# Performance work log

Measured on AMD Instinct MI355X. Metric: run time of the kernel, lower is better.

The kernel has to match this reference:

```python
import jax, jax.numpy as jnp
import numpy as np

N, E, V, H, HEADS, L, B = 20000, 320000, 100, 128, 3, 2, 200
NEG = 0.2   # leaky_relu negative_slope
EPS = 1e-5  # LayerNorm eps


def _mean_nodes(x, gid):
    # dgl.mean_nodes: per-graph mean of node features
    s = jax.ops.segment_sum(x, gid, num_segments=B)
    c = jax.ops.segment_sum(jnp.ones((x.shape[0], 1), x.dtype), gid, num_segments=B)
    return s / jnp.maximum(c, 1.0)


def _gat_layer(h, src, dst, Wn, bn, att, Ws, b, gamma, beta):
    # weight_node: Linear(H, H*HEADS)
    wv = (h @ Wn + bn).reshape(-1, HEADS, H)
    u = wv[src]  # [E, heads, H] gathered src features
    # attn = leaky_relu(sum(cat(u, v) * w_att)) split into u/v halves (no concat materialized)
    attn = (jnp.einsum('ehd,hd->eh', u, att[:, :H])
            + jnp.einsum('ehd,hd->eh', wv[dst], att[:, H:]))
    attn = jax.nn.leaky_relu(attn, NEG)  # [E, heads]
    # segment softmax over incoming edges of each dst node (mailbox softmax)
    m = jax.ops.segment_max(attn, dst, num_segments=N)
    m = jnp.where(jnp.isfinite(m), m, 0.0)
    e = jnp.exp(attn - m[dst])
    s = jax.ops.segment_sum(e, dst, num_segments=N)
    score = e / s[dst]
    agg = jax.ops.segment_sum(score[:, :, None] * u, dst, num_segments=N)  # [N, heads, H]
    res = agg.reshape(-1, HEADS * H) @ Ws + b
    # DGL leaves zero-in-degree nodes with zero reduced features (reduce_func never runs)
    has_in = jax.ops.segment_sum(jnp.ones((E,), h.dtype), dst, num_segments=N) > 0
    res = jnp.where(has_in[:, None], res, 0.0)
    x = res + h  # residual, then LayerNorm, relu (dropout is eval-mode identity)
    mu = jnp.mean(x, -1, keepdims=True)
    var = jnp.var(x, -1, keepdims=True)
    x = (x - mu) * jax.lax.rsqrt(var + EPS) * gamma + beta
    return jax.nn.relu(x)


def _gru_dir(x, Wih, Whh, bih, bhh, reverse):
    # torch nn.GRU single direction; x: [B, T, in]
    def step(hprev, xt):
        gi = xt @ Wih.T + bih
        gh = hprev @ Whh.T + bhh
        ir, iz, inn = jnp.split(gi, 3, -1)
        hr, hz, hn = jnp.split(gh, 3, -1)
        r = jax.nn.sigmoid(ir + hr)
        z = jax.nn.sigmoid(iz + hz)
        n = jnp.tanh(inn + r * hn)
        hnew = (1.0 - z) * n + z * hprev
        return hnew, hnew
    h0 = jnp.zeros((x.shape[0], Whh.shape[1]), x.dtype)
    hT, ys = jax.lax.scan(step, h0, jnp.swapaxes(x, 0, 1), reverse=reverse)
    return jnp.swapaxes(ys, 0, 1), hT


def setup_inputs() -> dict:
    key = jax.random.key(0)
    k = jax.random.split(key, 16)
    sc = 0.05
    return {
        'h': jax.random.normal(k[0], (N, H), jnp.float32),
        'wid': jax.random.randint(k[1], (N,), 0, V),
        'src': jax.random.randint(k[2], (E,), 0, N),
        'dst': jax.random.randint(k[3], (E,), 0, N),
        'graph_ids': jnp.sort(jax.random.randint(k[4], (N,), 0, B)),
        'proj_W': jax.random.normal(k[5], (V + H, H), jnp.float32) * sc,
        'proj_b': jnp.zeros((H,), jnp.float32),
        'conv_Wn': jax.random.normal(k[6], (L, H, HEADS * H), jnp.float32) * sc,
        'conv_bn': jnp.zeros((L, HEADS * H), jnp.float32),
        'conv_att': jax.random.normal(k[7], (L, HEADS, 2 * H), jnp.float32) * sc,
        'conv_Ws': jax.random.normal(k[8], (L, HEADS * H, H), jnp.float32) * sc,
        'conv_b': jnp.zeros((L, H), jnp.float32),
        'conv_gamma': jnp.ones((L, H), jnp.float32),
        'conv_beta': jnp.zeros((L, H), jnp.float32),
        'gru_Wih0': jax.random.normal(k[9], (2, 3 * H, H), jnp.float32) * sc,
        'gru_Whh0': jax.random.normal(k[10], (2, 3 * H, H), jnp.float32) * sc,
        'gru_bih0': jnp.zeros((2, 3 * H), jnp.float32),
        'gru_bhh0': jnp.zeros((2, 3 * H), jnp.float32),
        'gru_Wih1': jax.random.normal(k[11], (2, 3 * H, 2 * H), jnp.float32) * sc,
        'gru_Whh1': jax.random.normal(k[12], (2, 3 * H, H), jnp.float32) * sc,
        'gru_bih1': jnp.zeros((2, 3 * H), jnp.float32),
        'gru_bhh1': jnp.zeros((2, 3 * H), jnp.float32),
    }


def reference(h, wid, src, dst, graph_ids, proj_W, proj_b, conv_Wn, conv_bn, conv_att, conv_Ws, conv_b, conv_gamma, conv_beta, gru_Wih0, gru_Whh0, gru_bih0, gru_bhh0, gru_Wih1, gru_Whh1, gru_bih1, gru_bhh1):
    one_hot = jax.nn.one_hot(wid, V, dtype=h.dtype)
    hcur = jnp.concatenate([one_hot, h], -1) @ proj_W + proj_b  # project
    readouts = [_mean_nodes(hcur, graph_ids)]
    for l in range(L):
        hcur = _gat_layer(hcur, src, dst, conv_Wn[l], conv_bn[l], conv_att[l],
                          conv_Ws[l], conv_b[l], conv_gamma[l], conv_beta[l])
        readouts.append(_mean_nodes(hcur, graph_ids))
    x = jnp.stack(readouts, 1)  # [B, L+1, H] GRU readout sequence
    finals = []
    for (Wih, Whh, bih, bhh) in ((gru_Wih0, gru_Whh0, gru_bih0, gru_bhh0),
                                 (gru_Wih1, gru_Whh1, gru_bih1, gru_bhh1)):
        yf, hf = _gru_dir(x, Wih[0], Whh[0], bih[0], bhh[0], False)
        yb, hb = _gru_dir(x, Wih[1], Whh[1], bih[1], bhh[1], True)
        x = jnp.concatenate([yf, yb], -1)
        finals += [hf, hb]
    # torch returns h_n [num_layers*2, B, H]; module takes mean over dim 0
    return jnp.mean(jnp.stack(finals, 0), 0)  # [B, H]
```

## Files before the change

kernel.cpp:

```cpp
#include <hip/hip_runtime.h>
#include <cstddef>

static constexpr int Nn    = 20000;
static constexpr int Ee    = 320000;
static constexpr int Vv    = 100;
static constexpr int Hh    = 128;
static constexpr int HEADS = 3;
static constexpr int Bb    = 200;
static constexpr float NEG = 0.2f;
static constexpr float EPS = 1e-5f;

typedef short bf16x8 __attribute__((ext_vector_type(8)));
typedef float f32x4  __attribute__((ext_vector_type(4)));

__device__ inline unsigned short bf16_rne(float x) {
    unsigned u = __builtin_bit_cast(unsigned, x);
    u += 0x7FFFu + ((u >> 16) & 1u);
    return (unsigned short)(u >> 16);
}
__device__ inline float bf16_f(unsigned short h) {
    unsigned u = ((unsigned)h) << 16;
    return __builtin_bit_cast(float, u);
}
__device__ inline float bf_lo(unsigned u) { return __builtin_bit_cast(float, u << 16); }
__device__ inline float bf_hi(unsigned u) { return __builtin_bit_cast(float, u & 0xFFFF0000u); }
__device__ inline float lrelu(float a) { return a >= 0.f ? a : NEG * a; }
__device__ inline float sigmoidf(float x) { return 1.f / (1.f + __expf(-x)); }

__global__ void hist_dst(const int* __restrict__ dst, int* __restrict__ deg) {
    for (int i = blockIdx.x * blockDim.x + threadIdx.x; i < Ee; i += gridDim.x * blockDim.x)
        atomicAdd(&deg[dst[i]], 1);
}

__global__ __launch_bounds__(1024) void scan_offsets(const int* __restrict__ deg,
                                                     int* __restrict__ offs,
                                                     int* __restrict__ cur) {
    __shared__ int sums[1024];
    const int tid = threadIdx.x;
    const int per = (Nn + 1023) >> 10;
    int begin = tid * per;
    int end = begin + per; if (end > Nn) end = Nn;
    if (begin > Nn) begin = Nn;
    int s = 0;
    for (int i = begin; i < end; i++) s += deg[i];
    sums[tid] = s;
    __syncthreads();
    for (int off = 1; off < 1024; off <<= 1) {
// ... 7 lines not shown
        offs[i] = run; cur[i] = run;
        run += deg[i];
    }
    if (end == Nn) offs[Nn] = run;
}

__global__ void fill_csr(const int* __restrict__ dst, const int* __restrict__ src,
                         int* __restrict__ cur, int* __restrict__ csrc) {
    for (int i = blockIdx.x * blockDim.x + threadIdx.x; i < Ee; i += gridDim.x * blockDim.x) {
        int p = atomicAdd(&cur[dst[i]], 1);
        csrc[p] = src[i];
    }
}

struct PrepArgs {
    const float *projW, *convWn, *convWs, *Wih0, *Whh0, *Wih1, *Whh1;
    const int* gid;
    unsigned short *pBth, *pBtl;
    unsigned short *WnTh0, *WnTl0, *WnTh1, *WnTl1;
    unsigned short *WsTh0, *WsTl0, *WsTh1, *WsTl1;
    float *WihT0, *WhhT0, *WihT1, *WhhT1;
    int* goffs;
};

__device__ inline void wsplit(const float* B, int K, int N, int idx,
                              unsigned short* Bth, unsigned short* Btl) {
    int k = idx / N, n = idx - k * N;
    float v = B[idx];
    unsigned short h = bf16_rne(v);
    unsigned short l = bf16_rne(v - bf16_f(h));
    Bth[(size_t)n * K + k] = h;
    Btl[(size_t)n * K + k] = l;
}
__device__ inline void gruT(const float* W, int K, int idx, float* WT) {
    int d = idx / (384 * K);
    int r = idx - d * 384 * K;
    int j = r / K, k = r - j * K;
    WT[(size_t)d * K * 384 + (size_t)k * 384 + j] = W[idx];
}

__global__ void prep_all(PrepArgs a) {
    int i = blockIdx.x * blockDim.x + threadIdx.x;
    if (i < 16384)  { wsplit(a.projW, 128, 128, i, a.pBth, a.pBtl); return; }   i -= 16384;
    if (i < 49152)  { wsplit(a.convWn, 128, 384, i, a.WnTh0, a.WnTl0); return; } i -= 49152;
    if (i < 49152)  { wsplit(a.convWn + 49152, 128, 384, i, a.WnTh1, a.WnTl1); return; } i -= 49152;
    if (i < 49152)  { wsplit(a.convWs, 384, 128, i, a.WsTh0, a.WsTl0); return; } i -= 49152;
    if (i < 49152)  { wsplit(a.convWs + 49152, 384, 128, i, a.WsTh1, a.WsTl1); return; } i -= 49152;
    if (i < 98304)  { gruT(a.Wih0, 128, i, a.WihT0); return; }  i -= 98304;
    if (i < 98304)  { gruT(a.Whh0, 128, i, a.WhhT0); return; }  i -= 98304;
    if (i < 196608) { gruT(a.Wih1, 256, i, a.WihT1); return; }  i -= 196608;
    if (i < 98304)  { gruT(a.Whh1, 128, i, a.WhhT1); return; }  i -= 98304;
    if (i < Nn) {
        int g = a.gid[i];
        if (i == 0) { for (int b = 0; b <= g; b++) a.goffs[b] = 0; }
        else { int pg = a.gid[i - 1]; for (int b = pg + 1; b <= g; b++) a.goffs[b] = i; }
        if (i == Nn - 1) { for (int b = g + 1; b <= Bb; b++) a.goffs[b] = Nn; }
    }
}

struct GArgs {
    const float* A; const unsigned short* Bth; const unsigned short* Btl;
    const float* bias; int M, N, K;
    const int* wid; const float* projW;
    unsigned short* Cb; float* adf; float* addf; const float* att;
    const int* deg; const float* gamma; const float* beta;
    float* hcur;
    const int* gid; float* reado;
};

template <int MODE>
__global__ __launch_bounds__(256) void gemm_fused(GArgs a) {
    constexpr int WM = (MODE == 1) ? 2 : 1;
    constexpr int WN = 4 / WM;
    constexpr int MI = 2;
    constexpr int NI = (MODE == 1) ? 4 : 2;
    constexpr int BM = WM * MI * 16;
    __shared__ unsigned short As_hi[BM][40];
    __shared__ unsigned short As_lo[BM][40];
    __shared__ unsigned short Bs_hi[128][40];
    __shared__ unsigned short Bs_lo[128][40];
    const int tid  = threadIdx.x;
    const int row0 = blockIdx.y * BM;
    const int col0 = blockIdx.x * 128;
    const int w    = tid >> 6;
    const int wm   = w / WN;
    const int wn   = w % WN;
    const int L    = tid & 63;
    const int lrow = L & 15;
    const int lq   = L >> 4;
    const int M = a.M, N = a.N, K = a.K;

    f32x4 acc[MI][NI];
#pragma unroll
    for (int i = 0; i < MI; i++)
#pragma unroll
        for (int j = 0; j < NI; j++) acc[i][j] = (f32x4){0.f, 0.f, 0.f, 0.f};

    for (int kb = 0; kb < K; kb += 32) {
#pragma unroll
        for (int it = 0; it < BM / 32; it++) {
            int idx = tid + it * 256;
            int m  = idx >> 3;
            int kq = (idx & 7) * 4;
            int gr = row0 + m;
            float4 v = make_float4(0.f, 0.f, 0.f, 0.f);
            if (gr < M) v = *(const float4*)(a.A + (size_t)gr * K + kb + kq);
            unsigned short h0 = bf16_rne(v.x), h1 = bf16_rne(v.y),
                           h2 = bf16_rne(v.z), h3 = bf16_rne(v.w);
            short4 hi4 = make_short4((short)h0, (short)h1, (short)h2, (short)h3);
            short4 lo4 = make_short4((short)bf16_rne(v.x - bf16_f(h0)),
                                     (short)bf16_rne(v.y - bf16_f(h1)),
                                     (short)bf16_rne(v.z - bf16_f(h2)),
                                     (short)bf16_rne(v.w - bf16_f(h3)));
            *(short4*)&As_hi[m][kq] = hi4;
            *(short4*)&As_lo[m][kq] = lo4;
        }
        {
            int n  = tid >> 1;
            int kh = (tid & 1) * 16;
            const unsigned short* sh = a.Bth + (size_t)(col0 + n) * K + kb + kh;
            const unsigned short* sl = a.Btl + (size_t)(col0 + n) * K + kb + kh;
            *(float4*)&Bs_hi[n][kh]     = *(const float4*)sh;
            *(float4*)&Bs_hi[n][kh + 8] = *(const float4*)(sh + 8);
            *(float4*)&Bs_lo[n][kh]     = *(const float4*)sl;
            *(float4*)&Bs_lo[n][kh + 8] = *(const float4*)(sl + 8);
        }
        __syncthreads();
        bf16x8 ah[MI], al[MI], bh[NI], bl[NI];
#pragma unroll
        for (int mi = 0; mi < MI; mi++) {
            int r = wm * 32 + mi * 16 + lrow;
            ah[mi] = *(const bf16x8*)&As_hi[r][lq * 8];
            al[mi] = *(const bf16x8*)&As_lo[r][lq * 8];
        }
#pragma unroll
        for (int ni = 0; ni < NI; ni++) {
            int r = wn * NI * 16 + ni * 16 + lrow;
            bh[ni] = *(const bf16x8*)&Bs_hi[r][lq * 8];
            bl[ni] = *(const bf16x8*)&Bs_lo[r][lq * 8];
        }
#pragma unroll
        for (int mi = 0; mi < MI; mi++)
#pragma unroll
            for (int ni = 0; ni < NI; ni++) {
                acc[mi][ni] = __builtin_amdgcn_mfma_f32_16x16x32_bf16(ah[mi], bh[ni], acc[mi][ni], 0, 0, 0);
                acc[mi][ni] = __builtin_amdgcn_mfma_f32_16x16x32_bf16(ah[mi], bl[ni], acc[mi][ni], 0, 0, 0);
                acc[mi][ni] = __builtin_amdgcn_mfma_f32_16x16x32_bf16(al[mi], bh[ni], acc[mi][ni], 0, 0, 0);
            }
        __syncthreads();
    }

    float b4[NI];
#pragma unroll
    for (int ni = 0; ni < NI; ni++)
        b4[ni] = a.bias ? a.bias[col0 + wn * NI * 16 + ni * 16 + lrow] : 0.f;
#pragma unroll
    for (int mi = 0; mi < MI; mi++)
#pragma unroll
        for (int ni = 0; ni < NI; ni++)
#pragma unroll
            for (int r = 0; r < 4; r++) acc[mi][ni][r] += b4[ni];

    if constexpr (MODE == 0) {
        __shared__ float ytile[32][132];
        __shared__ int sgid[32];
#pragma unroll
        for (int mi = 0; mi < MI; mi++)
#pragma unroll
            for (int r = 0; r < 4; r++) {
                int lr = mi * 16 + lq * 4 + r;
                int row = row0 + lr;
                int wi = a.wid[row];
#pragma unroll
                for (int ni = 0; ni < NI; ni++) {
                    int c = wn * 32 + ni * 16 + lrow;
                    float y = acc[mi][ni][r] + a.projW[(size_t)wi * 128 + c];
                    a.hcur[(size_t)row * 128 + c] = y;
                    ytile[lr][c] = y;
                }
            }
        if (tid < 32) sgid[tid] = a.gid[row0 + tid];
        __syncthreads();
        int j = tid & 127, hh = tid >> 7;
        float sum = 0.f; int curg = -1;
        for (int r = hh * 16; r < hh * 16 + 16; r++) {
            int g = sgid[r];
            if (g != curg) {
                if (curg >= 0) atomicAdd(&a.reado[(size_t)curg * 128 + j], sum);
                sum = 0.f; curg = g;
            }
            sum += ytile[r][j];
        }
        if (curg >= 0) atomicAdd(&a.reado[(size_t)curg * 128 + j], sum);
    }

    if constexpr (MODE == 1) {
#pragma unroll
        for (int mi = 0; mi < MI; mi++)
#pragma unroll
            for (int ni = 0; ni < NI; ni++) {
                int col = col0 + wn * 64 + ni * 16 + lrow;
#pragma unroll
                for (int r = 0; r < 4; r++) {
                    int row = row0 + wm * 32 + mi * 16 + lq * 4 + r;
                    if (row < M) a.Cb[(size_t)row * N + col] = bf16_rne(acc[mi][ni][r]);
                }
            }
        const int h = blockIdx.x;
        const float* attS = a.att + h * 256;
        const float* attD = attS + 128;
        __shared__ float sred[64][2], dred[64][2];
        float as4[NI], ad4[NI];
#pragma unroll
        for (int ni = 0; ni < NI; ni++) {
            int cl = wn * 64 + ni * 16 + lrow;
            as4[ni] = attS[cl]; ad4[ni] = attD[cl];
        }
#pragma unroll
        for (int mi = 0; mi < MI; mi++)
#pragma unroll
            for (int r = 0; r < 4; r++) {
                float ps = 0.f, pd = 0.f;
#pragma unroll
                for (int ni = 0; ni < NI; ni++) {
                    ps += acc[mi][ni][r] * as4[ni];
                    pd += acc[mi][ni][r] * ad4[ni];
                }
#pragma unroll
                for (int o = 1; o < 16; o <<= 1) {
                    ps += __shfl_xor(ps, o, 64);
                    pd += __shfl_xor(pd, o, 64);
                }
                if (lrow == 0) {
                    int lr = wm * 32 + mi * 16 + lq * 4 + r;
                    sred[lr][wn] = ps; dred[lr][wn] = pd;
                }
            }
        __syncthreads();
        if (tid < 64) {
            int row = row0 + tid;
            if (row < M) {
                a.adf[(size_t)row * 4 + h]  = sred[tid][0] + sred[tid][1];
                a.addf[(size_t)row * 4 + h] = dred[tid][0] + dred[tid][1];
            }
        }
    }

    if constexpr (MODE == 2) {
        __shared__ float red1[32][4], red2[32][4];
        __shared__ float ytile[32][132];
        __shared__ int sgid[32];
        float g4[NI], be4[NI];
#pragma unroll
        for (int ni = 0; ni < NI; ni++) {
            int c = wn * 32 + ni * 16 + lrow;
            g4[ni] = a.gamma[c]; be4[ni] = a.beta[c];
        }
#pragma unroll
        for (int mi = 0; mi < MI; mi++)
#pragma unroll
            for (int r = 0; r < 4; r++) {
                int lr = mi * 16 + lq * 4 + r;
                int row = row0 + lr;
                int dg = a.deg[row];
#pragma unroll
                for (int ni = 0; ni < NI; ni++) {
                    int c = wn * 32 + ni * 16 + lrow;
                    float hold = a.hcur[(size_t)row * 128 + c];
                    acc[mi][ni][r] = hold + (dg > 0 ? acc[mi][ni][r] : 0.f);
                }
            }
#pragma unroll
        for (int mi = 0; mi < MI; mi++)
#pragma unroll
            for (int r = 0; r < 4; r++) {
                float ps = acc[mi][0][r] + acc[mi][1][r];
#pragma unroll
                for (int o = 1; o < 16; o <<= 1) ps += __shfl_xor(ps, o, 64);
                if (lrow == 0) red1[mi * 16 + lq * 4 + r][wn] = ps;
            }
        __syncthreads();
#pragma unroll
        for (int mi = 0; mi < MI; mi++)
#pragma unroll
            for (int r = 0; r < 4; r++) {
                int lr = mi * 16 + lq * 4 + r;
                float mu = (red1[lr][0] + red1[lr][1] + red1[lr][2] + red1[lr][3]) * (1.f / 128.f);
                float qs = 0.f;
#pragma unroll
                for (int ni = 0; ni < NI; ni++) {
                    float dx = acc[mi][ni][r] - mu;
                    qs += dx * dx;
                }
#pragma unroll
                for (int o = 1; o < 16; o <<= 1) qs += __shfl_xor(qs, o, 64);
                if (lrow == 0) red2[lr][wn] = qs;
            }
        __syncthreads();
#pragma unroll
        for (int mi = 0; mi < MI; mi++)
#pragma unroll
            for (int r = 0; r < 4; r++) {
                int lr = mi * 16 + lq * 4 + r;
                int row = row0 + lr;
                float mu = (red1[lr][0] + red1[lr][1] + red1[lr][2] + red1[lr][3]) * (1.f / 128.f);
                float var = (red2[lr][0] + red2[lr][1] + red2[lr][2] + red2[lr][3]) * (1.f / 128.f);
                float rs = rsqrtf(var + EPS);
#pragma unroll
                for (int ni = 0; ni < NI; ni++) {
                    int c = wn * 32 + ni * 16 + lrow;
                    float y = fmaxf((acc[mi][ni][r] - mu) * rs * g4[ni] + be4[ni], 0.f);
                    a.hcur[(size_t)row * 128 + c] = y;
                    ytile[lr][c] = y;
                }
            }
        if (tid < 32) sgid[tid] = a.gid[row0 + tid];
        __syncthreads();
        int j = tid & 127, hh = tid >> 7;
        float sum = 0.f; int curg = -1;
        for (int r = hh * 16; r < hh * 16 + 16; r++) {
            int g = sgid[r];
            if (g != curg) {
                if (curg >= 0) atomicAdd(&a.reado[(size_t)curg * 128 + j], sum);
                sum = 0.f; curg = g;
            }
            sum += ytile[r][j];
        }
        if (curg >= 0) atomicAdd(&a.reado[(size_t)curg * 128 + j], sum);
    }
}

__global__ __launch_bounds__(256) void gat_aggregate(const unsigned short* __restrict__ wv,
                                                     const float4* __restrict__ ad,
                                                     const float4* __restrict__ add,
                                                     const int* __restrict__ offs,
                                                     const int* __restrict__ csrc,
                                                     float* __restrict__ agg) {
    const int n = (blockIdx.x * 256 + threadIdx.x) >> 6;
    const int L = threadIdx.x & 63;
    if (n >= Nn) return;
    const int start = offs[n];
    const int deg = offs[n + 1] - start;
    float2* o2 = (float2*)(agg + (size_t)n * 384);
    if (deg == 0) {
        float2 z = make_float2(0.f, 0.f);
        o2[L] = z; o2[64 + L] = z; o2[128 + L] = z;
        return;
    }
    const float4 adn = add[n];
    float m0 = -1e30f, m1 = -1e30f, m2 = -1e30f;
    float s0 = 0.f, s1 = 0.f, s2 = 0.f;
    for (int i = L; i < deg; i += 64) {
        int sn = csrc[start + i];
        float4 a4 = ad[sn];
        float a0 = lrelu(a4.x + adn.x);
        float a1 = lrelu(a4.y + adn.y);
        float a2 = lrelu(a4.z + adn.z);
        float nm;
        nm = fmaxf(m0, a0); s0 = s0 * __expf(m0 - nm) + __expf(a0 - nm); m0 = nm;
        nm = fmaxf(m1, a1); s1 = s1 * __expf(m1 - nm) + __expf(a1 - nm); m1 = nm;
        nm = fmaxf(m2, a2); s2 = s2 * __expf(m2 - nm) + __expf(a2 - nm); m2 = nm;
    }
#pragma unroll
    for (int o = 32; o > 0; o >>= 1) {
        float om, os, nm;
        om = __shfl_xor(m0, o, 64); os = __shfl_xor(s0, o, 64);
        nm = fmaxf(m0, om); s0 = s0 * __expf(m0 - nm) + os * __expf(om - nm); m0 = nm;
        om = __shfl_xor(m1, o, 64); os = __shfl_xor(s1, o, 64);
        nm = fmaxf(m1, om); s1 = s1 * __expf(m1 - nm) + os * __expf(om - nm); m1 = nm;
        om = __shfl_xor(m2, o, 64); os = __shfl_xor(s2, o, 64);
        nm = fmaxf(m2, om); s2 = s2 * __expf(m2 - nm) + os * __expf(om - nm); m2 = nm;
    }
    const float i0 = 1.f / s0, i1 = 1.f / s1, i2 = 1.f / s2;
    float2 acc0 = make_float2(0.f, 0.f), acc1 = acc0, acc2 = acc0;
    for (int base = 0; base < deg; base += 64) {
        int cnt = deg - base; if (cnt > 64) cnt = 64;
        int sn = 0; float c0 = 0.f, c1 = 0.f, c2 = 0.f;
        if (L < cnt) {
            sn = csrc[start + base + L];
            float4 a4 = ad[sn];
            c0 = __expf(lrelu(a4.x + adn.x) - m0) * i0;
            c1 = __expf(lrelu(a4.y + adn.y) - m1) * i1;
            c2 = __expf(lrelu(a4.z + adn.z) - m2) * i2;
        }
        for (int j = 0; j < cnt; j++) {
            int    s_n = __shfl(sn, j, 64);
            float  w0  = __shfl(c0, j, 64);
            float  w1  = __shfl(c1, j, 64);
            float  w2  = __shfl(c2, j, 64);
            const unsigned* r2 = (const unsigned*)(wv + (size_t)s_n * 384);
            unsigned u0 = r2[L], u1 = r2[64 + L], u2 = r2[128 + L];
            acc0.x += w0 * bf_lo(u0); acc0.y += w0 * bf_hi(u0);
            acc1.x += w1 * bf_lo(u1); acc1.y += w1 * bf_hi(u1);
            acc2.x += w2 * bf_lo(u2); acc2.y += w2 * bf_hi(u2);
        }
    }
    o2[L] = acc0; o2[64 + L] = acc1; o2[128 + L] = acc2;
}

__global__ __launch_bounds__(768) void gru_all(const float* __restrict__ reado,
                                               const int* __restrict__ goffs,
                                               const float* __restrict__ WihT0,
                                               const float* __restrict__ WhhT0,
                                               const float* __restrict__ bih0,
                                               const float* __restrict__ bhh0,
                                               const float* __restrict__ WihT1,
                                               const float* __restrict__ WhhT1,
                                               const float* __restrict__ bih1,
                                               const float* __restrict__ bhh1,
                                               float* __restrict__ out) {
    const int b = blockIdx.x;
    const int tid = threadIdx.x;
// ... 93 lines not shown
    const float* convWs = (const float*)d_in[10];
    const float* convB  = (const float*)d_in[11];
    const float* convG  = (const float*)d_in[12];
    const float* convBe = (const float*)d_in[13];
    const float* Wih0   = (const float*)d_in[14];
    const float* Whh0   = (const float*)d_in[15];
    const float* bih0   = (const float*)d_in[16];
    const float* bhh0   = (const float*)d_in[17];
    const float* Wih1   = (const float*)d_in[18];
    const float* Whh1   = (const float*)d_in[19];
    const float* bih1   = (const float*)d_in[20];
    const float* bhh1   = (const float*)d_in[21];
    float* out = (float*)d_out;

    char* p = (char*)d_ws;
    auto alloc_f = [&](size_t n) { float* r = (float*)p; p += n * sizeof(float); return r; };
    auto alloc_i = [&](size_t n) { int* r = (int*)p; p += n * sizeof(int); return r; };
    auto alloc_s = [&](size_t n) { unsigned short* r = (unsigned short*)p; p += n * sizeof(unsigned short); return r; };
    float* hcur  = alloc_f((size_t)Nn * Hh);
    float* agg   = alloc_f((size_t)Nn * 384);
    float* adbuf = alloc_f((size_t)Nn * 4);
    float* addbuf= alloc_f((size_t)Nn * 4);
    float* reado = alloc_f((size_t)3 * Bb * Hh);
    int* deg  = alloc_i(Nn);
    const size_t zero_bytes = (size_t)3 * Bb * Hh * sizeof(float) + Nn * sizeof(int);
    float* WihT0 = alloc_f((size_t)2 * 128 * 384);
    float* WhhT0 = alloc_f((size_t)2 * 128 * 384);
    float* WihT1 = alloc_f((size_t)2 * 256 * 384);
    float* WhhT1 = alloc_f((size_t)2 * 128 * 384);
    int* offs = alloc_i(Nn + 1);
    int* cur  = alloc_i(Nn);
    int* csrc = alloc_i(Ee);
    int* goffs = alloc_i(Bb + 1);
    unsigned short* wv = alloc_s((size_t)Nn * 384);
    unsigned short* pBth  = alloc_s(128 * 128);
    unsigned short* pBtl  = alloc_s(128 * 128);
    unsigned short* WnTh[2] = { alloc_s(384 * 128), alloc_s(384 * 128) };
    unsigned short* WnTl[2] = { alloc_s(384 * 128), alloc_s(384 * 128) };
    unsigned short* WsTh[2] = { alloc_s(128 * 384), alloc_s(128 * 384) };
    unsigned short* WsTl[2] = { alloc_s(128 * 384), alloc_s(128 * 384) };

    hipMemsetAsync(reado, 0, zero_bytes, stream);

    hist_dst<<<1250, 256, 0, stream>>>(dst, deg);
    scan_offsets<<<1, 1024, 0, stream>>>(deg, offs, cur);
    fill_csr<<<1250, 256, 0, stream>>>(dst, src, cur, csrc);

    PrepArgs pa;
    pa.projW = projW + (size_t)Vv * Hh; pa.convWn = convWn; pa.convWs = convWs;
    pa.Wih0 = Wih0; pa.Whh0 = Whh0; pa.Wih1 = Wih1; pa.Whh1 = Whh1;
    pa.gid = gid;
    pa.pBth = pBth; pa.pBtl = pBtl;
    pa.WnTh0 = WnTh[0]; pa.WnTl0 = WnTl[0]; pa.WnTh1 = WnTh[1]; pa.WnTl1 = WnTl[1];
    pa.WsTh0 = WsTh[0]; pa.WsTl0 = WsTl[0]; pa.WsTh1 = WsTh[1]; pa.WsTl1 = WsTl[1];
    pa.WihT0 = WihT0; pa.WhhT0 = WhhT0; pa.WihT1 = WihT1; pa.WhhT1 = WhhT1;
    pa.goffs = goffs;
    prep_all<<<(724512 + 255) / 256, 256, 0, stream>>>(pa);

    {
        GArgs g = {};
        g.A = h; g.Bth = pBth; g.Btl = pBtl; g.bias = projB;
        g.M = Nn; g.N = 128; g.K = 128;
        g.wid = wid; g.projW = projW; g.hcur = hcur;
        g.gid = gid; g.reado = reado;
        gemm_fused<0><<<dim3(1, Nn / 32), 256, 0, stream>>>(g);
    }

    const int nwaveblocks = (Nn * 64 + 255) / 256;
    for (int l = 0; l < 2; l++) {
        {
            GArgs g = {};
            g.A = hcur; g.Bth = WnTh[l]; g.Btl = WnTl[l]; g.bias = convBn + l * 384;
            g.M = Nn; g.N = 384; g.K = 128;
            g.Cb = wv; g.adf = adbuf; g.addf = addbuf;
            g.att = convAtt + (size_t)l * 3 * 256;
            gemm_fused<1><<<dim3(3, (Nn + 63) / 64), 256, 0, stream>>>(g);
        }
        gat_aggregate<<<nwaveblocks, 256, 0, stream>>>(wv, (const float4*)adbuf, (const float4*)addbuf,
                                                       offs, csrc, agg);
        {
            GArgs g = {};
            g.A = agg; g.Bth = WsTh[l]; g.Btl = WsTl[l]; g.bias = convB + l * Hh;
            g.M = Nn; g.N = 128; g.K = 384;
            g.deg = deg; g.gamma = convG + l * Hh; g.beta = convBe + l * Hh;
            g.hcur = hcur;
            g.gid = gid; g.reado = reado + (size_t)(l + 1) * Bb * Hh;
            gemm_fused<2><<<dim3(1, Nn / 32), 256, 0, stream>>>(g);
        }
    }

    gru_all<<<Bb, 768, 0, stream>>>(reado, goffs, WihT0, WhhT0, bih0, bhh0,
                                    WihT1, WhhT1, bih1, bhh1, out);
}
```

Before: 415.5 us.

## Fold Wn into Ws and aggregate raw node features instead of projected heads

The per-layer projection Wn is algebraically folded into Ws: the GAT layer now aggregates softmax-weighted raw node features (bf16, 128 wide) per head, then applies one fused GEMM with precomputed Wn·Ws weights and a combined bias. Attention logits come from precomputed Wn·att vectors inside the previous GEMM's epilogue, which removes the 384-wide projection GEMM and the 384-wide bf16 gather per edge. The degree histogram is also merged into the prep kernel, cutting one launch. In exchange, prep does more work computing the fused weights, and the different summation order may change rounding.

Result: faster. 377.0 us (-9.3%).

```diff
diff --git a/kernel.cpp b/kernel.cpp
--- a/kernel.cpp
+++ b/kernel.cpp
@@ -1,5 +1,6 @@
 #include <hip/hip_runtime.h>
 #include <cstddef>
+#include <cstdint>
 
 static constexpr int Nn    = 20000;
 static constexpr int Ee    = 320000;
@@ -26,11 +27,6 @@
 __device__ inline float bf_hi(unsigned u) { return __builtin_bit_cast(float, u & 0xFFFF0000u); }
 __device__ inline float lrelu(float a) { return a >= 0.f ? a : NEG * a; }
 __device__ inline float sigmoidf(float x) { return 1.f / (1.f + __expf(-x)); }
-
-__global__ void hist_dst(const int* __restrict__ dst, int* __restrict__ deg) {
-    for (int i = blockIdx.x * blockDim.x + threadIdx.x; i < Ee; i += gridDim.x * blockDim.x)
-        atomicAdd(&deg[dst[i]], 1);
-}
 
 __global__ __launch_bounds__(1024) void scan_offsets(const int* __restrict__ deg,
                                                      int* __restrict__ offs,
@@ -68,13 +64,14 @@
 }
 
 struct PrepArgs {
-    const float *projW, *convWn, *convWs, *Wih0, *Whh0, *Wih1, *Whh1;
-    const int* gid;
+    const float *projW, *convWn, *convWs, *convAtt, *convBn, *convB;
+    const float *Wih0, *Whh0, *Wih1, *Whh1;
+    const int *gid, *dst;
     unsigned short *pBth, *pBtl;
-    unsigned short *WnTh0, *WnTl0, *WnTh1, *WnTl1;
-    unsigned short *WsTh0, *WsTl0, *WsTh1, *WsTl1;
+    unsigned short *WfTh0, *WfTl0, *WfTh1, *WfTl1;
+    float *vavd, *vc, *biasF;
     float *WihT0, *WhhT0, *WihT1, *WhhT1;
-    int* goffs;
+    int *goffs, *deg;
 };
 
 __device__ inline void wsplit(const float* B, int K, int N, int idx,
@@ -95,11 +92,54 @@
 
 __global__ void prep_all(PrepArgs a) {
     int i = blockIdx.x * blockDim.x + threadIdx.x;
-    if (i < 16384)  { wsplit(a.projW, 128, 128, i, a.pBth, a.pBtl); return; }   i -= 16384;
-    if (i < 49152)  { wsplit(a.convWn, 128, 384, i, a.WnTh0, a.WnTl0); return; } i -= 49152;
-    if (i < 49152)  { wsplit(a.convWn + 49152, 128, 384, i, a.WnTh1, a.WnTl1); return; } i -= 49152;
-    if (i < 49152)  { wsplit(a.convWs, 384, 128, i, a.WsTh0, a.WsTl0); return; } i -= 49152;
-    if (i < 49152)  { wsplit(a.convWs + 49152, 384, 128, i, a.WsTh1, a.WsTl1); return; } i -= 49152;
+    if (i < 16384) { wsplit(a.projW, 128, 128, i, a.pBth, a.pBtl); return; } i -= 16384;
+#pragma unroll
+    for (int l = 0; l < 2; l++) {
+        if (i < 49152) {
+            int k = i >> 7, c = i & 127;
+            int h = k >> 7, i_ = k & 127;
+            const float* wn = a.convWn + (size_t)l * 49152 + (size_t)i_ * 384 + h * 128;
+            const float* ws = a.convWs + (size_t)l * 49152 + (size_t)(h * 128) * 128 + c;
+            float v = 0.f;
+            for (int j = 0; j < 128; j++) v += wn[j] * ws[(size_t)j * 128];
+            unsigned short hi = bf16_rne(v);
+            unsigned short lo = bf16_rne(v - bf16_f(hi));
+            unsigned short* th = l ? a.WfTh1 : a.WfTh0;
+            unsigned short* tl = l ? a.WfTl1 : a.WfTl0;
+            th[(size_t)c * 384 + k] = hi;
+            tl[(size_t)c * 384 + k] = lo;
+            return;
+        }
+        i -= 49152;
+    }
+    if (i < 1536) {
+        int l = i / 768, r = i % 768;
+        int sd = r / 384, rr = r % 384, h = rr >> 7, i_ = rr & 127;
+        const float* wn = a.convWn + (size_t)l * 49152 + (size_t)i_ * 384 + h * 128;
+        const float* at = a.convAtt + l * 768 + h * 256 + sd * 128;
+        float v = 0.f;
+        for (int j = 0; j < 128; j++) v += wn[j] * at[j];
+        a.vavd[i] = v;
+        return;
+    } i -= 1536;
+    if (i < 12) {
+        int l = i / 6, r = i % 6, sd = r / 3, h = r % 3;
+        const float* bn = a.convBn + l * 384 + h * 128;
+        const float* at = a.convAtt + l * 768 + h * 256 + sd * 128;
+        float v = 0.f;
+        for (int j = 0; j < 128; j++) v += bn[j] * at[j];
+        a.vc[i] = v;
+        return;
+    } i -= 12;
+    if (i < 256) {
+        int l = i >> 7, c = i & 127;
+        const float* bn = a.convBn + l * 384;
+        const float* ws = a.convWs + (size_t)l * 49152 + c;
+        float v = a.convB[l * 128 + c];
+        for (int k = 0; k < 384; k++) v += bn[k] * ws[(size_t)k * 128];
+        a.biasF[i] = v;
+        return;
+    } i -= 256;
     if (i < 98304)  { gruT(a.Wih0, 128, i, a.WihT0); return; }  i -= 98304;
     if (i < 98304)  { gruT(a.Whh0, 128, i, a.WhhT0); return; }  i -= 98304;
     if (i < 196608) { gruT(a.Wih1, 256, i, a.WihT1); return; }  i -= 196608;
@@ -109,94 +149,86 @@
         if (i == 0) { for (int b = 0; b <= g; b++) a.goffs[b] = 0; }
         else { int pg = a.gid[i - 1]; for (int b = pg + 1; b <= g; b++) a.goffs[b] = i; }
         if (i == Nn - 1) { for (int b = g + 1; b <= Bb; b++) a.goffs[b] = Nn; }
-    }
+        return;
+    } i -= Nn;
+    if (i < Ee) atomicAdd(&a.deg[a.dst[i]], 1);
 }
 
 struct GArgs {
     const float* A; const unsigned short* Bth; const unsigned short* Btl;
-    const float* bias; int M, N, K;
+    const float* bias; int M, K;
     const int* wid; const float* projW;
-    unsigned short* Cb; float* adf; float* addf; const float* att;
     const int* deg; const float* gamma; const float* beta;
     float* hcur;
     const int* gid; float* reado;
+    const float* vavd; const float* vc;
+    float* adf; float* addf;
+    unsigned short* hb;
 };
 
 template <int MODE>
 __global__ __launch_bounds__(256) void gemm_fused(GArgs a) {
-    constexpr int WM = (MODE == 1) ? 2 : 1;
-    constexpr int WN = 4 / WM;
-    constexpr int MI = 2;
-    constexpr int NI = (MODE == 1) ? 4 : 2;
-    constexpr int BM = WM * MI * 16;
-    __shared__ unsigned short As_hi[BM][40];
-    __shared__ unsigned short As_lo[BM][40];
+    __shared__ unsigned short As_hi[32][40];
+    __shared__ unsigned short As_lo[32][40];
     __shared__ unsigned short Bs_hi[128][40];
     __shared__ unsigned short Bs_lo[128][40];
+    __shared__ float ytile[32][132];
+    __shared__ int sgid[32];
     const int tid  = threadIdx.x;
-    const int row0 = blockIdx.y * BM;
-    const int col0 = blockIdx.x * 128;
-    const int w    = tid >> 6;
-    const int wm   = w / WN;
-    const int wn   = w % WN;
+    const int row0 = blockIdx.y * 32;
+    const int wn   = tid >> 6;
     const int L    = tid & 63;
     const int lrow = L & 15;
     const int lq   = L >> 4;
-    const int M = a.M, N = a.N, K = a.K;
-
-    f32x4 acc[MI][NI];
-#pragma unroll
-    for (int i = 0; i < MI; i++)
-#pragma unroll
-        for (int j = 0; j < NI; j++) acc[i][j] = (f32x4){0.f, 0.f, 0.f, 0.f};
+    const int K = a.K;
+
+    f32x4 acc[2][2];
+#pragma unroll
+    for (int i = 0; i < 2; i++)
+#pragma unroll
+        for (int j = 0; j < 2; j++) acc[i][j] = (f32x4){0.f, 0.f, 0.f, 0.f};
 
     for (int kb = 0; kb < K; kb += 32) {
-#pragma unroll
-        for (int it = 0; it < BM / 32; it++) {
-            int idx = tid + it * 256;
-            int m  = idx >> 3;
-            int kq = (idx & 7) * 4;
-            int gr = row0 + m;
-            float4 v = make_float4(0.f, 0.f, 0.f, 0.f);
-            if (gr < M) v = *(const float4*)(a.A + (size_t)gr * K + kb + kq);
+        {
+            int m  = tid >> 3;
+            int kq = (tid & 7) * 4;
+            float4 v = *(const float4*)(a.A + (size_t)(row0 + m) * K + kb + kq);
             unsigned short h0 = bf16_rne(v.x), h1 = bf16_rne(v.y),
                            h2 = bf16_rne(v.z), h3 = bf16_rne(v.w);
-            short4 hi4 = make_short4((short)h0, (short)h1, (short)h2, (short)h3);
-            short4 lo4 = make_short4((short)bf16_rne(v.x - bf16_f(h0)),
-                                     (short)bf16_rne(v.y - bf16_f(h1)),
-                                     (short)bf16_rne(v.z - bf16_f(h2)),
-                                     (short)bf16_rne(v.w - bf16_f(h3)));
-            *(short4*)&As_hi[m][kq] = hi4;
-            *(short4*)&As_lo[m][kq] = lo4;
+            *(short4*)&As_hi[m][kq] = make_short4((short)h0, (short)h1, (short)h2, (short)h3);
+            *(short4*)&As_lo[m][kq] = make_short4((short)bf16_rne(v.x - bf16_f(h0)),
+                                                  (short)bf16_rne(v.y - bf16_f(h1)),
+                                                  (short)bf16_rne(v.z - bf16_f(h2)),
+                                                  (short)bf16_rne(v.w - bf16_f(h3)));
         }
         {
             int n  = tid >> 1;
             int kh = (tid & 1) * 16;
-            const unsigned short* sh = a.Bth + (size_t)(col0 + n) * K + kb + kh;
-            const unsigned short* sl = a.Btl + (size_t)(col0 + n) * K + kb + kh;
+            const unsigned short* sh = a.Bth + (size_t)n * K + kb + kh;
+            const unsigned short* sl = a.Btl + (size_t)n * K + kb + kh;
             *(float4*)&Bs_hi[n][kh]     = *(const float4*)sh;
             *(float4*)&Bs_hi[n][kh + 8] = *(const float4*)(sh + 8);
             *(float4*)&Bs_lo[n][kh]     = *(const float4*)sl;
             *(float4*)&Bs_lo[n][kh + 8] = *(const float4*)(sl + 8);
         }
         __syncthreads();
-        bf16x8 ah[MI], al[MI], bh[NI], bl[NI];
-#pragma unroll
-        for (int mi = 0; mi < MI; mi++) {
-            int r = wm * 32 + mi * 16 + lrow;
+        bf16x8 ah[2], al[2], bh[2], bl[2];
+#pragma unroll
+        for (int mi = 0; mi < 2; mi++) {
+            int r = mi * 16 + lrow;
             ah[mi] = *(const bf16x8*)&As_hi[r][lq * 8];
             al[mi] = *(const bf16x8*)&As_lo[r][lq * 8];
         }
 #pragma unroll
-        for (int ni = 0; ni < NI; ni++) {
-            int r = wn * NI * 16 + ni * 16 + lrow;
+        for (int ni = 0; ni < 2; ni++) {
+            int r = wn * 32 + ni * 16 + lrow;
             bh[ni] = *(const bf16x8*)&Bs_hi[r][lq * 8];
             bl[ni] = *(const bf16x8*)&Bs_lo[r][lq * 8];
         }
 #pragma unroll
-        for (int mi = 0; mi < MI; mi++)
-#pragma unroll
-            for (int ni = 0; ni < NI; ni++) {
+        for (int mi = 0; mi < 2; mi++)
+#pragma unroll
+            for (int ni = 0; ni < 2; ni++) {
                 acc[mi][ni] = __builtin_amdgcn_mfma_f32_16x16x32_bf16(ah[mi], bh[ni], acc[mi][ni], 0, 0, 0);
                 acc[mi][ni] = __builtin_amdgcn_mfma_f32_16x16x32_bf16(ah[mi], bl[ni], acc[mi][ni], 0, 0, 0);
                 acc[mi][ni] = __builtin_amdgcn_mfma_f32_16x16x32_bf16(al[mi], bh[ni], acc[mi][ni], 0, 0, 0);
@@ -204,37 +236,105 @@
         __syncthreads();
     }
 
-    float b4[NI];
-#pragma unroll
-    for (int ni = 0; ni < NI; ni++)
-        b4[ni] = a.bias ? a.bias[col0 + wn * NI * 16 + ni * 16 + lrow] : 0.f;
-#pragma unroll
-    for (int mi = 0; mi < MI; mi++)
-#pragma unroll
-        for (int ni = 0; ni < NI; ni++)
-#pragma unroll
-            for (int r = 0; r < 4; r++) acc[mi][ni][r] += b4[ni];
+#pragma unroll
+    for (int ni = 0; ni < 2; ni++) {
+        float bb = a.bias[wn * 32 + ni * 16 + lrow];
+#pragma unroll
+        for (int mi = 0; mi < 2; mi++)
+#pragma unroll
+            for (int r = 0; r < 4; r++) acc[mi][ni][r] += bb;
+    }
 
     if constexpr (MODE == 0) {
-        __shared__ float ytile[32][132];
-        __shared__ int sgid[32];
-#pragma unroll
-        for (int mi = 0; mi < MI; mi++)
+#pragma unroll
+        for (int mi = 0; mi < 2; mi++)
 #pragma unroll
             for (int r = 0; r < 4; r++) {
                 int lr = mi * 16 + lq * 4 + r;
                 int row = row0 + lr;
                 int wi = a.wid[row];
 #pragma unroll
-                for (int ni = 0; ni < NI; ni++) {
+                for (int ni = 0; ni < 2; ni++) {
                     int c = wn * 32 + ni * 16 + lrow;
                     float y = acc[mi][ni][r] + a.projW[(size_t)wi * 128 + c];
                     a.hcur[(size_t)row * 128 + c] = y;
                     ytile[lr][c] = y;
                 }
             }
-        if (tid < 32) sgid[tid] = a.gid[row0 + tid];
+    }
+
+    if constexpr (MODE == 2) {
+        __shared__ float red1[32][4], red2[32][4];
+        float g4[2], be4[2];
+#pragma unroll
+        for (int ni = 0; ni < 2; ni++) {
+            int c = wn * 32 + ni * 16 + lrow;
+            g4[ni] = a.gamma[c]; be4[ni] = a.beta[c];
+        }
+#pragma unroll
+        for (int mi = 0; mi < 2; mi++)
+#pragma unroll
+            for (int r = 0; r < 4; r++) {
+                int lr = mi * 16 + lq * 4 + r;
+                int row = row0 + lr;
+                int dg = a.deg[row];
+#pragma unroll
+                for (int ni = 0; ni < 2; ni++) {
+                    int c = wn * 32 + ni * 16 + lrow;
+                    float hold = a.hcur[(size_t)row * 128 + c];
+                    acc[mi][ni][r] = hold + (dg > 0 ? acc[mi][ni][r] : 0.f);
+                }
+            }
+#pragma unroll
+        for (int mi = 0; mi < 2; mi++)
+#pragma unroll
+            for (int r = 0; r < 4; r++) {
+                float ps = acc[mi][0][r] + acc[mi][1][r];
+#pragma unroll
+                for (int o = 1; o < 16; o <<= 1) ps += __shfl_xor(ps, o, 64);
+                if (lrow == 0) red1[mi * 16 + lq * 4 + r][wn] = ps;
+            }
         __syncthreads();
+#pragma unroll
+        for (int mi = 0; mi < 2; mi++)
+#pragma unroll
+            for (int r = 0; r < 4; r++) {
+                int lr = mi * 16 + lq * 4 + r;
+                float mu = (red1[lr][0] + red1[lr][1] + red1[lr][2] + red1[lr][3]) * (1.f / 128.f);
+                float qs = 0.f;
+#pragma unroll
+                for (int ni = 0; ni < 2; ni++) {
+                    float dx = acc[mi][ni][r] - mu;
+                    qs += dx * dx;
+                }
+#pragma unroll
+                for (int o = 1; o < 16; o <<= 1) qs += __shfl_xor(qs, o, 64);
+                if (lrow == 0) red2[lr][wn] = qs;
+            }
+        __syncthreads();
+#pragma unroll
+        for (int mi = 0; mi < 2; mi++)
+#pragma unroll
+            for (int r = 0; r < 4; r++) {
+                int lr = mi * 16 + lq * 4 + r;
+                int row = row0 + lr;
+                float mu = (red1[lr][0] + red1[lr][1] + red1[lr][2] + red1[lr][3]) * (1.f / 128.f);
+                float var = (red2[lr][0] + red2[lr][1] + red2[lr][2] + red2[lr][3]) * (1.f / 128.f);
+                float rs = rsqrtf(var + EPS);
+#pragma unroll
+                for (int ni = 0; ni < 2; ni++) {
+                    int c = wn * 32 + ni * 16 + lrow;
+                    float y = fmaxf((acc[mi][ni][r] - mu) * rs * g4[ni] + be4[ni], 0.f);
+                    a.hcur[(size_t)row * 128 + c] = y;
+                    ytile[lr][c] = y;
+                }
+            }
+    }
+
+    if (tid < 32) sgid[tid] = a.gid[row0 + tid];
+    __syncthreads();
+
+    {
         int j = tid & 127, hh = tid >> 7;
         float sum = 0.f; int curg = -1;
         for (int r = hh * 16; r < hh * 16 + 16; r++) {
@@ -248,208 +348,122 @@
         if (curg >= 0) atomicAdd(&a.reado[(size_t)curg * 128 + j], sum);
     }
 
-    if constexpr (MODE == 1) {
-#pragma unroll
-        for (int mi = 0; mi < MI; mi++)
-#pragma unroll
-            for (int ni = 0; ni < NI; ni++) {
-                int col = col0 + wn * 64 + ni * 16 + lrow;
-#pragma unroll
-                for (int r = 0; r < 4; r++) {
-                    int row = row0 + wm * 32 + mi * 16 + lq * 4 + r;
-                    if (row < M) a.Cb[(size_t)row * N + col] = bf16_rne(acc[mi][ni][r]);
-                }
-            }
-        const int h = blockIdx.x;
-        const float* attS = a.att + h * 256;
-        const float* attD = attS + 128;
-        __shared__ float sred[64][2], dred[64][2];
-        float as4[NI], ad4[NI];
-#pragma unroll
-        for (int ni = 0; ni < NI; ni++) {
-            int cl = wn * 64 + ni * 16 + lrow;
-            as4[ni] = attS[cl]; ad4[ni] = attD[cl];
-        }
-#pragma unroll
-        for (int mi = 0; mi < MI; mi++)
-#pragma unroll
-            for (int r = 0; r < 4; r++) {
-                float ps = 0.f, pd = 0.f;
-#pragma unroll
-                for (int ni = 0; ni < NI; ni++) {
-                    ps += acc[mi][ni][r] * as4[ni];
-                    pd += acc[mi][ni][r] * ad4[ni];
-                }
-#pragma unroll
-                for (int o = 1; o < 16; o <<= 1) {
-                    ps += __shfl_xor(ps, o, 64);
-                    pd += __shfl_xor(pd, o, 64);
-                }
-                if (lrow == 0) {
-                    int lr = wm * 32 + mi * 16 + lq * 4 + r;
-                    sred[lr][wn] = ps; dred[lr][wn] = pd;
-                }
-            }
-        __syncthreads();
-        if (tid < 64) {
-            int row = row0 + tid;
-            if (row < M) {
-                a.adf[(size_t)row * 4 + h]  = sred[tid][0] + sred[tid][1];
-                a.addf[(size_t)row * 4 + h] = dred[tid][0] + dred[tid][1];
-            }
-        }
-    }
-
-    if constexpr (MODE == 2) {
-        __shared__ float red1[32][4], red2[32][4];
-        __shared__ float ytile[32][132];
-        __shared__ int sgid[32];
-        float g4[NI], be4[NI];
-#pragma unroll
-        for (int ni = 0; ni < NI; ni++) {
-            int c = wn * 32 + ni * 16 + lrow;
-            g4[ni] = a.gamma[c]; be4[ni] = a.beta[c];
-        }
-#pragma unroll
-        for (int mi = 0; mi < MI; mi++)
-#pragma unroll
-            for (int r = 0; r < 4; r++) {
-                int lr = mi * 16 + lq * 4 + r;
-                int row = row0 + lr;
-                int dg = a.deg[row];
-#pragma unroll
-                for (int ni = 0; ni < NI; ni++) {
-                    int c = wn * 32 + ni * 16 + lrow;
-                    float hold = a.hcur[(size_t)row * 128 + c];
-                    acc[mi][ni][r] = hold + (dg > 0 ? acc[mi][ni][r] : 0.f);
-                }
-            }
-#pragma unroll
-        for (int mi = 0; mi < MI; mi++)
-#pragma unroll
-            for (int r = 0; r < 4; r++) {
-                float ps = acc[mi][0][r] + acc[mi][1][r];
-#pragma unroll
-                for (int o = 1; o < 16; o <<= 1) ps += __shfl_xor(ps, o, 64);
-                if (lrow == 0) red1[mi * 16 + lq * 4 + r][wn] = ps;
-            }
-        __syncthreads();
-#pragma unroll
-        for (int mi = 0; mi < MI; mi++)
-#pragma unroll
-            for (int r = 0; r < 4; r++) {
-                int lr = mi * 16 + lq * 4 + r;
-                float mu = (red1[lr][0] + red1[lr][1] + red1[lr][2] + red1[lr][3]) * (1.f / 128.f);
-                float qs = 0.f;
-#pragma unroll
-                for (int ni = 0; ni < NI; ni++) {
-                    float dx = acc[mi][ni][r] - mu;
-                    qs += dx * dx;
-                }
-#pragma unroll
-                for (int o = 1; o < 16; o <<= 1) qs += __shfl_xor(qs, o, 64);
-                if (lrow == 0) red2[lr][wn] = qs;
-            }
-        __syncthreads();
-#pragma unroll
-        for (int mi = 0; mi < MI; mi++)
-#pragma unroll
-            for (int r = 0; r < 4; r++) {
-                int lr = mi * 16 + lq * 4 + r;
-                int row = row0 + lr;
-                float mu = (red1[lr][0] + red1[lr][1] + red1[lr][2] + red1[lr][3]) * (1.f / 128.f);
-                float var = (red2[lr][0] + red2[lr][1] + red2[lr][2] + red2[lr][3]) * (1.f / 128.f);
-                float rs = rsqrtf(var + EPS);
-#pragma unroll
-                for (int ni = 0; ni < NI; ni++) {
-                    int c = wn * 32 + ni * 16 + lrow;
-                    float y = fmaxf((acc[mi][ni][r] - mu) * rs * g4[ni] + be4[ni], 0.f);
-                    a.hcur[(size_t)row * 128 + c] = y;
-                    ytile[lr][c] = y;
-                }
-            }
-        if (tid < 32) sgid[tid] = a.gid[row0 + tid];
-        __syncthreads();
-        int j = tid & 127, hh = tid >> 7;
-        float sum = 0.f; int curg = -1;
-        for (int r = hh * 16; r < hh * 16 + 16; r++) {
-            int g = sgid[r];
-            if (g != curg) {
-                if (curg >= 0) atomicAdd(&a.reado[(size_t)curg * 128 + j], sum);
-                sum = 0.f; curg = g;
-            }
-            sum += ytile[r][j];
-        }
-        if (curg >= 0) atomicAdd(&a.reado[(size_t)curg * 128 + j], sum);
-    }
-}
-
-__global__ __launch_bounds__(256) void gat_aggregate(const unsigned short* __restrict__ wv,
-                                                     const float4* __restrict__ ad,
-                                                     const float4* __restrict__ add,
-                                                     const int* __restrict__ offs,
-                                                     const int* __restrict__ csrc,
-                                                     float* __restrict__ agg) {
+    if (a.vavd) {
+        int row = tid & 31, which = tid >> 5;
+        if (which < 6) {
+            const float* v = a.vavd + which * 128;
+            float s = 0.f;
+            for (int c = 0; c < 128; c++) s += ytile[row][c] * v[c];
+            s += a.vc[which];
+            int node = row0 + row;
+            int sd = which / 3, h = which - sd * 3;
+            float* dstp = sd ? a.addf : a.adf;
+            dstp[(size_t)node * 4 + h] = s;
+        }
+        {
+            int row = tid >> 3, c0 = (tid & 7) * 16;
+            unsigned* dst = (unsigned*)(a.hb + (size_t)(row0 + row) * 128 + c0);
+#pragma unroll
+            for (int q = 0; q < 8; q++) {
+                unsigned lo = bf16_rne(ytile[row][c0 + 2 * q]);
+                unsigned hi = bf16_rne(ytile[row][c0 + 2 * q + 1]);
+                dst[q] = lo | (hi << 16);
+            }
+        }
+    }
+}
+
+__global__ __launch_bounds__(256) void gat_gather(const unsigned short* __restrict__ hb,
+                                                  const float4* __restrict__ ad,
+                                                  const float4* __restrict__ add,
+                                                  const int* __restrict__ offs,
+                                                  const int* __restrict__ csrc,
+                                                  float* __restrict__ T) {
+    __shared__ float4 slot[4][64];
     const int n = (blockIdx.x * 256 + threadIdx.x) >> 6;
+    const int wv_ = threadIdx.x >> 6;
     const int L = threadIdx.x & 63;
     if (n >= Nn) return;
     const int start = offs[n];
     const int deg = offs[n + 1] - start;
-    float2* o2 = (float2*)(agg + (size_t)n * 384);
+    float2* o2 = (float2*)(T + (size_t)n * 384);
     if (deg == 0) {
         float2 z = make_float2(0.f, 0.f);
         o2[L] = z; o2[64 + L] = z; o2[128 + L] = z;
         return;
     }
     const float4 adn = add[n];
-    float m0 = -1e30f, m1 = -1e30f, m2 = -1e30f;
-    float s0 = 0.f, s1 = 0.f, s2 = 0.f;
-    for (int i = L; i < deg; i += 64) {
-        int sn = csrc[start + i];
-        float4 a4 = ad[sn];
-        float a0 = lrelu(a4.x + adn.x);
-        float a1 = lrelu(a4.y + adn.y);
-        float a2 = lrelu(a4.z + adn.z);
-        float nm;
-        nm = fmaxf(m0, a0); s0 = s0 * __expf(m0 - nm) + __expf(a0 - nm); m0 = nm;
-        nm = fmaxf(m1, a1); s1 = s1 * __expf(m1 - nm) + __expf(a1 - nm); m1 = nm;
-        nm = fmaxf(m2, a2); s2 = s2 * __expf(m2 - nm) + __expf(a2 - nm); m2 = nm;
-    }
-#pragma unroll
-    for (int o = 32; o > 0; o >>= 1) {
-        float om, os, nm;
-        om = __shfl_xor(m0, o, 64); os = __shfl_xor(s0, o, 64);
-        nm = fmaxf(m0, om); s0 = s0 * __expf(m0 - nm) + os * __expf(om - nm); m0 = nm;
-        om = __shfl_xor(m1, o, 64); os = __shfl_xor(s1, o, 64);
-        nm = fmaxf(m1, om); s1 = s1 * __expf(m1 - nm) + os * __expf(om - nm); m1 = nm;
-        om = __shfl_xor(m2, o, 64); os = __shfl_xor(s2, o, 64);
-        nm = fmaxf(m2, om); s2 = s2 * __expf(m2 - nm) + os * __expf(om - nm); m2 = nm;
-    }
-    const float i0 = 1.f / s0, i1 = 1.f / s1, i2 = 1.f / s2;
-    float2 acc0 = make_float2(0.f, 0.f), acc1 = acc0, acc2 = acc0;
-    for (int base = 0; base < deg; base += 64) {
-        int cnt = deg - base; if (cnt > 64) cnt = 64;
-        int sn = 0; float c0 = 0.f, c1 = 0.f, c2 = 0.f;
-        if (L < cnt) {
-            sn = csrc[start + base + L];
+    float2 t0 = make_float2(0.f, 0.f), t1 = t0, t2 = t0;
+
+    if (deg <= 64) {
+        int sn = 0; float e0 = 0.f, e1 = 0.f, e2 = 0.f;
+        if (L < deg) {
+            sn = csrc[start + L];
             float4 a4 = ad[sn];
-            c0 = __expf(lrelu(a4.x + adn.x) - m0) * i0;
-            c1 = __expf(lrelu(a4.y + adn.y) - m1) * i1;
-            c2 = __expf(lrelu(a4.z + adn.z) - m2) * i2;
-        }
-        for (int j = 0; j < cnt; j++) {
-            int    s_n = __shfl(sn, j, 64);
-            float  w0  = __shfl(c0, j, 64);
-            float  w1  = __shfl(c1, j, 64);
-            float  w2  = __shfl(c2, j, 64);
-            const unsigned* r2 = (const unsigned*)(wv + (size_t)s_n * 384);
-            unsigned u0 = r2[L], u1 = r2[64 + L], u2 = r2[128 + L];
-            acc0.x += w0 * bf_lo(u0); acc0.y += w0 * bf_hi(u0);
-            acc1.x += w1 * bf_lo(u1); acc1.y += w1 * bf_hi(u1);
-            acc2.x += w2 * bf_lo(u2); acc2.y += w2 * bf_hi(u2);
-        }
-    }
-    o2[L] = acc0; o2[64 + L] = acc1; o2[128 + L] = acc2;
+            e0 = __expf(lrelu(a4.x + adn.x));
+            e1 = __expf(lrelu(a4.y + adn.y));
+            e2 = __expf(lrelu(a4.z + adn.z));
+        }
+        float s0 = e0, s1 = e1, s2 = e2;
+#pragma unroll
+        for (int o = 32; o > 0; o >>= 1) {
+            s0 += __shfl_xor(s0, o, 64);
+            s1 += __shfl_xor(s1, o, 64);
+            s2 += __shfl_xor(s2, o, 64);
+        }
+        slot[wv_][L] = make_float4(__builtin_bit_cast(float, sn),
+                                   e0 / s0, e1 / s1, e2 / s2);
+        __builtin_amdgcn_wave_barrier();
+#pragma unroll 2
+        for (int j = 0; j < deg; j++) {
+            float4 sc = slot[wv_][j];
+            int s_n = __builtin_bit_cast(int, sc.x);
+            unsigned u = ((const unsigned*)(hb + (size_t)s_n * 128))[L];
+            float x0 = bf_lo(u), x1 = bf_hi(u);
+            t0.x += sc.y * x0; t0.y += sc.y * x1;
+            t1.x += sc.z * x0; t1.y += sc.z * x1;
+            t2.x += sc.w * x0; t2.y += sc.w * x1;
+        }
+    } else {
+        float s0 = 0.f, s1 = 0.f, s2 = 0.f;
+        for (int i = L; i < deg; i += 64) {
+            int sn = csrc[start + i];
+            float4 a4 = ad[sn];
+            s0 += __expf(lrelu(a4.x + adn.x));
+            s1 += __expf(lrelu(a4.y + adn.y));
+            s2 += __expf(lrelu(a4.z + adn.z));
+        }
+#pragma unroll
+        for (int o = 32; o > 0; o >>= 1) {
+            s0 += __shfl_xor(s0, o, 64);
+            s1 += __shfl_xor(s1, o, 64);
+            s2 += __shfl_xor(s2, o, 64);
+        }
+        float i0 = 1.f / s0, i1 = 1.f / s1, i2 = 1.f / s2;
+        for (int base = 0; base < deg; base += 64) {
+            int cnt = deg - base; if (cnt > 64) cnt = 64;
+            if (L < cnt) {
+                int sn = csrc[start + base + L];
+                float4 a4 = ad[sn];
+                slot[wv_][L] = make_float4(__builtin_bit_cast(float, sn),
+                                           __expf(lrelu(a4.x + adn.x)) * i0,
+                                           __expf(lrelu(a4.y + adn.y)) * i1,
+                                           __expf(lrelu(a4.z + adn.z)) * i2);
+            }
+            __builtin_amdgcn_wave_barrier();
+            for (int j = 0; j < cnt; j++) {
+                float4 sc = slot[wv_][j];
+                int s_n = __builtin_bit_cast(int, sc.x);
+                unsigned u = ((const unsigned*)(hb + (size_t)s_n * 128))[L];
+                float x0 = bf_lo(u), x1 = bf_hi(u);
+                t0.x += sc.y * x0; t0.y += sc.y * x1;
+                t1.x += sc.z * x0; t1.y += sc.z * x1;
+                t2.x += sc.w * x0; t2.y += sc.w * x1;
+            }
+            __builtin_amdgcn_wave_barrier();
+        }
+    }
+    o2[L] = t0; o2[64 + L] = t1; o2[128 + L] = t2;
 }
 
 __global__ __launch_bounds__(768) void gru_all(const float* __restrict__ reado,
@@ -573,11 +587,12 @@
     float* out = (float*)d_out;
 
     char* p = (char*)d_ws;
-    auto alloc_f = [&](size_t n) { float* r = (float*)p; p += n * sizeof(float); return r; };
-    auto alloc_i = [&](size_t n) { int* r = (int*)p; p += n * sizeof(int); return r; };
-    auto alloc_s = [&](size_t n) { unsigned short* r = (unsigned short*)p; p += n * sizeof(unsigned short); return r; };
-    float* hcur  = alloc_f((size_t)Nn * Hh);
-    float* agg   = alloc_f((size_t)Nn * 384);
+    auto align16 = [&]() { p = (char*)(((uintptr_t)p + 15) & ~(uintptr_t)15); };
+    auto alloc_f = [&](size_t n) { align16(); float* r = (float*)p; p += n * sizeof(float); return r; };
+    auto alloc_i = [&](size_t n) { align16(); int* r = (int*)p; p += n * sizeof(int); return r; };
+    auto alloc_s = [&](size_t n) { align16(); unsigned short* r = (unsigned short*)p; p += n * sizeof(unsigned short); return r; };
+    float* hcur  = alloc_f((size_t)Nn * 128);
+    float* T     = alloc_f((size_t)Nn * 384);
     float* adbuf = alloc_f((size_t)Nn * 4);
     float* addbuf= alloc_f((size_t)Nn * 4);
     float* reado = alloc_f((size_t)3 * Bb * Hh);
@@ -587,63 +602,60 @@
     float* WhhT0 = alloc_f((size_t)2 * 128 * 384);
     float* WihT1 = alloc_f((size_t)2 * 256 * 384);
     float* WhhT1 = alloc_f((size_t)2 * 128 * 384);
+    float* vavd  = alloc_f(1536);
+    float* vc    = alloc_f(12);
+    float* biasF = alloc_f(256);
     int* offs = alloc_i(Nn + 1);
     int* cur  = alloc_i(Nn);
     int* csrc = alloc_i(Ee);
     int* goffs = alloc_i(Bb + 1);
-    unsigned short* wv = alloc_s((size_t)Nn * 384);
-    unsigned short* pBth  = alloc_s(128 * 128);
-    unsigned short* pBtl  = alloc_s(128 * 128);
-    unsigned short* WnTh[2] = { alloc_s(384 * 128), alloc_s(384 * 128) };
-    unsigned short* WnTl[2] = { alloc_s(384 * 128), alloc_s(384 * 128) };
-    unsigned short* WsTh[2] = { alloc_s(128 * 384), alloc_s(128 * 384) };
-    unsigned short* WsTl[2] = { alloc_s(128 * 384), alloc_s(128 * 384) };
+    unsigned short* hb = alloc_s((size_t)Nn * 128);
+    unsigned short* pBth = alloc_s(128 * 128);
+    unsigned short* pBtl = alloc_s(128 * 128);
+    unsigned short* WfTh[2] = { alloc_s(128 * 384), alloc_s(128 * 384) };
+    unsigned short* WfTl[2] = { alloc_s(128 * 384), alloc_s(128 * 384) };
 
     hipMemsetAsync(reado, 0, zero_bytes, stream);
 
-    hist_dst<<<1250, 256, 0, stream>>>(dst, deg);
+    PrepArgs pa;
+    pa.projW = projW + (size_t)Vv * Hh;
+    pa.convWn = convWn; pa.convWs = convWs; pa.convAtt = convAtt;
+    pa.convBn = convBn; pa.convB = convB;
+    pa.Wih0 = Wih0; pa.Whh0 = Whh0; pa.Wih1 = Wih1; pa.Whh1 = Whh1;
+    pa.gid = gid; pa.dst = dst;
+    pa.pBth = pBth; pa.pBtl = pBtl;
+    pa.WfTh0 = WfTh[0]; pa.WfTl0 = WfTl[0]; pa.WfTh1 = WfTh[1]; pa.WfTl1 = WfTl[1];
+    pa.vavd = vavd; pa.vc = vc; pa.biasF = biasF;
+    pa.WihT0 = WihT0; pa.WhhT0 = WhhT0; pa.WihT1 = WihT1; pa.WhhT1 = WhhT1;
+    pa.goffs = goffs; pa.deg = deg;
+    const int prep_total = 16384 + 2 * 49152 + 1536 + 12 + 256 + 98304 + 98304 + 196608 + 98304 + Nn + Ee;
+    prep_all<<<(prep_total + 255) / 256, 256, 0, stream>>>(pa);
+
     scan_offsets<<<1, 1024, 0, stream>>>(deg, offs, cur);
     fill_csr<<<1250, 256, 0, stream>>>(dst, src, cur, csrc);
-
-    PrepArgs pa;
-    pa.projW = projW + (size_t)Vv * Hh; pa.convWn = convWn; pa.convWs = convWs;
-    pa.Wih0 = Wih0; pa.Whh0 = Whh0; pa.Wih1 = Wih1; pa.Whh1 = Whh1;
-    pa.gid = gid;
-    pa.pBth = pBth; pa.pBtl = pBtl;
-    pa.WnTh0 = WnTh[0]; pa.WnTl0 = WnTl[0]; pa.WnTh1 = WnTh[1]; pa.WnTl1 = WnTl[1];
-    pa.WsTh0 = WsTh[0]; pa.WsTl0 = WsTl[0]; pa.WsTh1 = WsTh[1]; pa.WsTl1 = WsTl[1];
-    pa.WihT0 = WihT0; pa.WhhT0 = WhhT0; pa.WihT1 = WihT1; pa.WhhT1 = WhhT1;
-    pa.goffs = goffs;
-    prep_all<<<(724512 + 255) / 256, 256, 0, stream>>>(pa);
 
     {
         GArgs g = {};
         g.A = h; g.Bth = pBth; g.Btl = pBtl; g.bias = projB;
-        g.M = Nn; g.N = 128; g.K = 128;
+        g.M = Nn; g.K = 128;
         g.wid = wid; g.projW = projW; g.hcur = hcur;
         g.gid = gid; g.reado = reado;
+        g.vavd = vavd; g.vc = vc; g.adf = adbuf; g.addf = addbuf; g.hb = hb;
         gemm_fused<0><<<dim3(1, Nn / 32), 256, 0, stream>>>(g);
     }
 
     const int nwaveblocks = (Nn * 64 + 255) / 256;
     for (int l = 0; l < 2; l++) {
+        gat_gather<<<nwaveblocks, 256, 0, stream>>>(hb, (const float4*)adbuf, (const float4*)addbuf,
+                                                    offs, csrc, T);
         {
             GArgs g = {};
-            g.A = hcur; g.Bth = WnTh[l]; g.Btl = WnTl[l]; g.bias = convBn + l * 384;
-            g.M = Nn; g.N = 384; g.K = 128;
-            g.Cb = wv; g.adf = adbuf; g.addf = addbuf;
-            g.att = convAtt + (size_t)l * 3 * 256;
-            gemm_fused<1><<<dim3(3, (Nn + 63) / 64), 256, 0, stream>>>(g);
-        }
-        gat_aggregate<<<nwaveblocks, 256, 0, stream>>>(wv, (const float4*)adbuf, (const float4*)addbuf,
-                                                       offs, csrc, agg);
-        {
-            GArgs g = {};
-            g.A = agg; g.Bth = WsTh[l]; g.Btl = WsTl[l]; g.bias = convB + l * Hh;
-            g.M = Nn; g.N = 128; g.K = 384;
+            g.A = T; g.Bth = WfTh[l]; g.Btl = WfTl[l]; g.bias = biasF + l * 128;
+            g.M = Nn; g.K = 384;
             g.deg = deg; g.gamma = convG + l * Hh; g.beta = convBe + l * Hh;
             g.hcur = hcur;
             g.gid = gid; g.reado = reado + (size_t)(l + 1) * Bb * Hh;
+            if (l == 0) { g.vavd = vavd + 768; g.vc = vc + 6; g.adf = adbuf; g.addf = addbuf; g.hb = hb; }
             gemm_fused<2><<<dim3(1, Nn / 32), 256, 0, stream>>>(g);
         }
     }
```
